# Kernel optimization log

Hardware: AMD Instinct MI355X
Metric: run time of the kernel (lower is better)

## Reference

```python
import jax, jax.numpy as jnp
import numpy as np

N_HEAD = 16


def _rope_tables(T, head_dim, dtype):
    # RotaryEmbedding buffers: freqs = outer(t, inv_freq), half-dim tables [T, head_dim//2]
    inv_freq = 1.0 / (10000.0 ** (jnp.arange(0, head_dim, 2, dtype=jnp.float32) / head_dim))
    freqs = jnp.arange(T, dtype=jnp.float32)[:, None] * inv_freq[None, :]
    return jnp.cos(freqs).astype(dtype), jnp.sin(freqs).astype(dtype)


def _apply_rotary(x, cos, sin):
    # x: [B,H,T,D]; cos/sin: [T,D//2] broadcast over B,H
    d = x.shape[-1] // 2
    x1, x2 = x[..., :d], x[..., d:]
    return jnp.concatenate([x1 * cos - x2 * sin, x2 * cos + x1 * sin], axis=-1)


def setup_inputs() -> dict:
    key = jax.random.key(0)
    k1, k2, k3 = jax.random.split(key, 3)
    B, T, C = 2, 2048, 2048
    x = jax.random.normal(k1, (B, T, C), dtype=jnp.float32)
    Wqkv = jax.random.normal(k2, (C, 3 * C), dtype=jnp.float32) * (1.0 / np.sqrt(C))
    Wproj = jax.random.normal(k3, (C, C), dtype=jnp.float32) * (1.0 / np.sqrt(C))
    return {"x": x, "Wqkv": Wqkv, "Wproj": Wproj}


def reference(x, Wqkv, Wproj):
    B, T, C = x.shape
    H = N_HEAD
    D = C // H
    qkv = (x @ Wqkv).reshape(B, T, 3, H, D)
    q, k, v = qkv[:, :, 0], qkv[:, :, 1], qkv[:, :, 2]  # [B,T,H,D]
    q = jnp.transpose(q, (0, 2, 1, 3))  # [B,H,T,D]
    k = jnp.transpose(k, (0, 2, 1, 3))
    v = jnp.transpose(v, (0, 2, 1, 3))
    cos, sin = _rope_tables(T, D, x.dtype)
    q = _apply_rotary(q, cos, sin)
    k = _apply_rotary(k, cos, sin)
    scale = 1.0 / np.sqrt(D)
    scores = jnp.einsum('bhqd,bhkd->bhqk', q, k) * scale
    causal = jnp.tril(jnp.ones((T, T), dtype=bool))
    scores = jnp.where(causal, scores, jnp.finfo(scores.dtype).min)
    attn = jax.nn.softmax(scores, axis=-1)
    out = jnp.einsum('bhqk,bhkd->bhqd', attn, v)
    out = jnp.transpose(out, (0, 2, 1, 3)).reshape(B, T, C)
    return out @ Wproj
```

## Files before the change

### kernel.cpp

```cpp
#include <hip/hip_runtime.h>
#include <hip/hip_bf16.h>

typedef short s16b;
using bf16x4 = __attribute__((ext_vector_type(4))) short;
using bf16x8 = __attribute__((ext_vector_type(8))) short;
using f32x4  = __attribute__((ext_vector_type(4))) float;

#define DEVINL __device__ __forceinline__

DEVINL float bf2f(short u) {
    union { float f; unsigned u; } x;
    x.u = ((unsigned)(unsigned short)u) << 16;
    return x.f;
}
DEVINL short f2bf(float f) {
    unsigned u = __builtin_bit_cast(unsigned, f);
    u += 0x7FFFu + ((u >> 16) & 1u);
    return (short)(u >> 16);
}

DEVINL f32x4 mfma16(bf16x8 a, bf16x8 b, f32x4 c) {
    return __builtin_amdgcn_mfma_f32_16x16x32_bf16(a, b, c, 0, 0, 0);
}

DEVINL void gload_lds16(const void* g, void* lds_uniform) {
    __builtin_amdgcn_global_load_lds(
        (const __attribute__((address_space(1))) char*)(const char*)g,
        (__attribute__((address_space(3))) char*)(char*)lds_uniform, 16, 0, 0);
}

DEVINL int perm32(int k) {
    return ((k >> 2) & 3) * 8 + ((k >> 4) & 1) * 4 + (k & 3);
}

DEVINL bf16x8 lds128(const s16b* base, int row, int ks, int g) {
    const char* p = (const char*)base + row * 128 + ((((ks << 2) + g) ^ (row & 7)) << 4);
    return *(const bf16x8*)p;
}
DEVINL bf16x8 lds256(const s16b* base, int row, int ds, int g) {
    const char* p = (const char*)base + row * 256 + ((((ds << 2) + g) ^ (row & 7)) << 4);
    return *(const bf16x8*)p;
}

__global__ void k_tables(float* __restrict__ ctab, float* __restrict__ stab) {
    int idx = blockIdx.x * 256 + threadIdx.x;
    int i = idx & 63, t = idx >> 6;
    float inv = powf(10000.0f, -(float)i * (1.0f / 64.0f));
    float fr = (float)t * inv;
    ctab[idx] = cosf(fr);
    stab[idx] = sinf(fr);
}

__global__ void k_cvt_x(const float* __restrict__ x, s16b* __restrict__ xb) {
    int idx = blockIdx.x * 256 + threadIdx.x;
    int p = idx * 4;
    int row = p >> 11, pc = p & 2047;
    int grp = pc >> 5, sp = pc & 31;
    int c = sp >> 3, half = (sp >> 2) & 1;
    int ksrc = grp * 32 + half * 16 + c * 4;
    float4 v = *(const float4*)(x + (size_t)row * 2048 + ksrc);
    bf16x4 o;
    o[0] = f2bf(v.x); o[1] = f2bf(v.y); o[2] = f2bf(v.z); o[3] = f2bf(v.w);
    *(bf16x4*)(xb + (size_t)row * 2048 + pc) = o;
}

__global__ void k_tcvt(const float* __restrict__ in, s16b* __restrict__ out, int R, int C) {
    __shared__ float tile[32][33];
    int tx = threadIdx.x & 31, ty = threadIdx.x >> 5;
    int c0 = blockIdx.x * 32, r0 = blockIdx.y * 32;
#pragma unroll
    for (int kk = 0; kk < 4; ++kk) {
        int r = ty + kk * 8;
        tile[r][tx] = in[(size_t)(r0 + r) * C + c0 + tx];
    }
    __syncthreads();
#pragma unroll
    for (int kk = 0; kk < 4; ++kk) {
        int r = ty + kk * 8;
        out[(size_t)(c0 + r) * R + r0 + perm32(tx)] = f2bf(tile[tx][r]);
    }
}

#define STG_B01(DB, KB)                                                        \
  gload_lds16(srcB + (KB), lds + 49152 + (DB) * 32768 + tid16);                \
  gload_lds16(srcB + 262144 + (KB), lds + 49152 + (DB) * 32768 + 8192 + tid16);
#define STG_B23(DB, KB)                                                        \
  gload_lds16(srcB + 524288 + (KB), lds + 49152 + (DB) * 32768 + 16384 + tid16); \
  gload_lds16(srcB + 786432 + (KB), lds + 49152 + (DB) * 32768 + 24576 + tid16);
#define STG_A01(DB, KB)                                                        \
  gload_lds16(srcA + (KB), lds + (DB) * 16384 + tid16);                        \
  gload_lds16(srcA + 262144 + (KB), lds + (DB) * 16384 + 8192 + tid16);

#define AF_READ(B, KS)                                                         \
    _Pragma("unroll")                                                          \
    for (int fi = 0; fi < 4; ++fi) {                                           \
      int row = (fi >> 1) * 64 + wm * 32 + (fi & 1) * 16 + r15;                \
      af[fi] = *(const bf16x8*)(lds + (B) * 16384 + row * 128                  \
               + ((((KS) * 4 + g) ^ (row & 7)) << 4));                         \
    }

#define PH4(B, KH, JH, STGC, WN)                                               \
  {                                                                            \
    if ((JH) == 0) { AF_READ(B, KH) }                                          \
    _Pragma("unroll")                                                          \
    for (int fj = 0; fj < 2; ++fj) {                                           \
      int row = (JH) * 128 + wn * 32 + fj * 16 + r15;                          \
      bfr[fj] = *(const bf16x8*)(lds + 49152 + (B) * 32768 + row * 128         \
                + ((((KH) * 4 + g) ^ (row & 7)) << 4));                        \
    }                                                                          \
    STGC                                                                       \
    if ((WN) == 6) { asm volatile("s_waitcnt vmcnt(6)" ::: "memory");          \
                     __builtin_amdgcn_sched_barrier(0); }                      \
    else if ((WN) == 0) { asm volatile("s_waitcnt vmcnt(0)" ::: "memory");     \
                     __builtin_amdgcn_sched_barrier(0); }                      \
    __builtin_amdgcn_s_barrier();                                              \
    asm volatile("s_waitcnt lgkmcnt(0)" ::: "memory");                         \
    __builtin_amdgcn_sched_barrier(0);                                         \
    __builtin_amdgcn_s_setprio(1);                                             \
    _Pragma("unroll")                                                          \
    for (int fi = 0; fi < 4; ++fi)                                             \
      _Pragma("unroll")                                                        \
      for (int fj = 0; fj < 2; ++fj)                                           \
        acc[fi][(JH) * 2 + fj] = mfma16(af[fi], bfr[fj], acc[fi][(JH) * 2 + fj]); \
    __builtin_amdgcn_s_setprio(0);                                             \
    __builtin_amdgcn_s_barrier();                                              \
    __builtin_amdgcn_sched_barrier(0);                                         \
  }

#define DO_TILE3(B, S1, S2, S3, WNL)                                           \
    PH4(B, 0, 0, S1, -1)                                                       \
    PH4(B, 0, 1, S2, -1)                                                       \
    PH4(B, 1, 0, S3, -1)                                                       \
    PH4(B, 1, 1, , WNL)

#define GEMM3_MAINLOOP(A_, B_)                                                 \
    __shared__ __attribute__((aligned(16))) char lds[147456];                  \
    const int tid = threadIdx.x;                                               \
    const int lane = tid & 63, wave = tid >> 6;                                \
    const int g = lane >> 4, r15 = lane & 15;                                  \
    const int wm = wave >> 2, wn = wave & 3;                                   \
    const int tid16 = tid << 4;                                                \
    const int rowL = tid16 >> 7;                                               \
    const int swzL = ((((tid16 >> 4) & 7) ^ (rowL & 7)) << 4);                 \
    const char* srcA = (const char*)(A_) + (size_t)(bm + rowL) * 4096 + swzL;  \
    const char* srcB = (const char*)(B_) + (size_t)(bn + rowL) * 4096 + swzL;  \
    f32x4 acc[4][4] = {};                                                      \
    bf16x8 af[4], bfr[2];                                                      \
    STG_B01(0, 0) STG_A01(0, 0) STG_B23(0, 0)                                  \
    STG_B01(1, 128) STG_A01(1, 128) STG_B23(1, 128)                            \
    asm volatile("s_waitcnt vmcnt(6)" ::: "memory");                           \
    __builtin_amdgcn_sched_barrier(0);                                         \
    __builtin_amdgcn_s_barrier();                                              \
    for (int t3 = 0; t3 < 10; ++t3) {                                          \
        const int kb2 = (3 * t3 + 2) * 128;                                    \
        const int kb3 = kb2 + 128, kb4 = kb2 + 256;                            \
        DO_TILE3(0, STG_B01(2, kb2), STG_A01(2, kb2), STG_B23(2, kb2), 6)      \
        DO_TILE3(1, STG_B01(0, kb3), STG_A01(0, kb3), STG_B23(0, kb3), 6)      \
        DO_TILE3(2, STG_B01(1, kb4), STG_A01(1, kb4), STG_B23(1, kb4), 6)      \
    }                                                                          \
    DO_TILE3(0, , , , 0)                                                       \
    DO_TILE3(1, , , , -1)

__global__ __launch_bounds__(512) void k_gemm_qkv(
    const s16b* __restrict__ A, const s16b* __restrict__ Bt,
    s16b* __restrict__ Qb, s16b* __restrict__ Kb, s16b* __restrict__ Vt) {
    const int bid = blockIdx.x;
    const int xcd = bid & 7, local = bid >> 3;
    const int rr_ = local >> 5, w = local & 31;
    const int bm = ((xcd & 3) * 8 + (w >> 2)) * 128;
    const int bn = ((xcd >> 2) * 12 + rr_ * 4 + (w & 3)) * 256;
    GEMM3_MAINLOOP(A, Bt)
    const int which = bn >> 11;
    if (which < 2) {
        s16b* dst = which ? Kb : Qb;
        char* sml = (char*)lds;
#pragma unroll
        for (int i = 0; i < 4; ++i) {
#pragma unroll
            for (int j = 0; j < 4; ++j) {
                int mb0 = (i >> 1) * 64 + wm * 32 + (i & 1) * 16 + 4 * g;
                int nn = (j >> 1) * 128 + wn * 32 + (j & 1) * 16 + r15;
#pragma unroll
                for (int e = 0; e < 4; ++e) {
                    int mm = mb0 + e;
                    *(s16b*)(sml + mm * 528 + ((nn * 2) ^ ((mm & 3) << 5))) =
                        f2bf(acc[i][j][e]);
                }
            }
        }
        __syncthreads();
        const int mrow = tid >> 2, c4 = tid & 3;
        const int bb = bm >> 11;
        const int tt = (bm & 2047) + mrow;
        const char* srow = sml + mrow * 528;
        const int sw = (mrow & 3) << 5;
#pragma unroll
        for (int k = 0; k < 8; ++k) {
            int lc = c4 + 4 * k;
            bf16x8 v = *(const bf16x8*)(srow + ((lc * 16) ^ sw));
            int ng = bn + lc * 8;
            int h = (ng >> 7) & 15, d = ng & 127;
            *(bf16x8*)(dst + ((size_t)(bb * 16 + h) * 2048 + tt) * 128 + d) = v;
        }
    } else {
#pragma unroll
        for (int i = 0; i < 4; ++i) {
            int m0 = bm + (i >> 1) * 64 + wm * 32 + (i & 1) * 16 + 4 * g;
            int b = m0 >> 11, t0 = m0 & 2047;
#pragma unroll
            for (int j = 0; j < 4; ++j) {
                int n = bn + (j >> 1) * 128 + wn * 32 + (j & 1) * 16 + r15;
                int h = (n >> 7) & 15, d = n & 127;
                size_t bh = (size_t)(b * 16 + h);
                int pt = (t0 & ~31) + perm32(t0 & 31);
                size_t base = (bh * 128 + d) * 2048 + pt;
                bf16x4 pk;
#pragma unroll
                for (int e = 0; e < 4; ++e) pk[e] = f2bf(acc[i][j][e]);
                *(bf16x4*)(Vt + base) = pk;
            }
        }
    }
}

__global__ __launch_bounds__(512) void k_gemm_proj(
    const s16b* __restrict__ A, const s16b* __restrict__ Bt, float* __restrict__ Co) {
    const int bid = blockIdx.x;
    const int xcd = bid & 7, local = bid >> 3;
    const int bm = (xcd * 4 + (local & 3)) * 128;
    const int bn = (local >> 2) * 256;
    GEMM3_MAINLOOP(A, Bt)
#pragma unroll
    for (int i = 0; i < 4; ++i) {
        int m0 = bm + (i >> 1) * 64 + wm * 32 + (i & 1) * 16 + 4 * g;
#pragma unroll
        for (int j = 0; j < 4; ++j) {
            int n = bn + (j >> 1) * 128 + wn * 32 + (j & 1) * 16 + r15;
#pragma unroll
            for (int e = 0; e < 4; ++e) Co[(size_t)(m0 + e) * 2048 + n] = acc[i][j][e];
        }
    }
}

__global__ void k_rope(s16b* __restrict__ Qb, const s16b* __restrict__ Kb,
                       s16b* __restrict__ Kp,
                       const float* __restrict__ ctab, const float* __restrict__ stab) {
    int idx = blockIdx.x * 256 + threadIdx.x;
    int i4 = idx & 15;
    int t = (idx >> 4) & 2047;
    int bh = (idx >> 15) & 31;
    int which = idx >> 20;
    int d = i4 * 4;
    const float* cp = ctab + t * 64 + d;
    const float* sp = stab + t * 64 + d;
    size_t rowoff = ((size_t)bh * 2048 + t) * 128;
    if (which == 0) {
        s16b* P = Qb + rowoff;
        bf16x4 a = *(bf16x4*)(P + d);
        bf16x4 bv = *(bf16x4*)(P + d + 64);
        bf16x4 ra, rb;
#pragma unroll
        for (int e = 0; e < 4; ++e) {
            float c = cp[e], s = sp[e];
            float x1 = bf2f(a[e]), x2 = bf2f(bv[e]);
            ra[e] = f2bf(x1 * c - x2 * s);
            rb[e] = f2bf(x2 * c + x1 * s);
        }
        *(bf16x4*)(P + d) = ra;
        *(bf16x4*)(P + d + 64) = rb;
    } else {
        const s16b* Pi = Kb + rowoff;
        s16b* Po = Kp + rowoff;
        bf16x4 a = *(const bf16x4*)(Pi + d);
        bf16x4 bv = *(const bf16x4*)(Pi + d + 64);
        bf16x4 ra, rb;
#pragma unroll
        for (int e = 0; e < 4; ++e) {
            float c = cp[e], s = sp[e];
            float x1 = bf2f(a[e]), x2 = bf2f(bv[e]);
            ra[e] = f2bf(x1 * c - x2 * s);
            rb[e] = f2bf(x2 * c + x1 * s);
        }
        int d2 = d + 64;
        int pd  = (d  & ~31) + perm32(d  & 31);
        int pd2 = (d2 & ~31) + perm32(d2 & 31);
        *(bf16x4*)(Po + pd) = ra;
        *(bf16x4*)(Po + pd2) = rb;
    }
}

__global__ __launch_bounds__(256) void k_attn(
    const s16b* __restrict__ Qb, const s16b* __restrict__ Kp,
    const s16b* __restrict__ Vt, s16b* __restrict__ AO) {
    __shared__ alignas(16) s16b Ks[64 * 128];
    __shared__ alignas(16) s16b Vs[128 * 64];
    const int tid = threadIdx.x;
    const int lane = tid & 63, wave = tid >> 6;
    const int g = lane >> 4, r15 = lane & 15;
    const int bh = blockIdx.x, qt = 15 - blockIdx.y;
    const int q0 = qt * 128 + wave * 32;
    const s16b* Qg = Qb + (size_t)bh * 2048 * 128;
    const char* Kg = (const char*)(Kp + (size_t)bh * 2048 * 128);
    const char* Vg = (const char*)(Vt + (size_t)bh * 128 * 2048);

    bf16x8 qf[2][4];
#pragma unroll
    for (int qs = 0; qs < 2; ++qs)
#pragma unroll
        for (int ds = 0; ds < 4; ++ds) {
            const s16b* p = Qg + (size_t)(q0 + qs * 16 + r15) * 128 + ds * 32 + 4 * g;
            bf16x4 lo = *(const bf16x4*)p;
            bf16x4 hi = *(const bf16x4*)(p + 16);
            qf[qs][ds] = __builtin_shufflevector(lo, hi, 0, 1, 2, 3, 4, 5, 6, 7);
        }

    f32x4 ot[8][2] = {};
    float m_s[2] = {-3e38f, -3e38f};
    float l_s[2] = {0.f, 0.f};
    const float scale = 0.0883883476483184f;

    const int ktiles = qt * 2 + 2;
    for (int kt = 0; kt < ktiles; ++kt) {
        const int k0 = kt * 64;
        __syncthreads();
#pragma unroll
        for (int rr = 0; rr < 4; ++rr) {
            int uo = (rr * 256 + wave * 64) * 16;
            int o = uo + lane * 16;
            {
                int row = o >> 8, sl = (o >> 4) & 15;
                int sg = (sl ^ (row & 7)) << 4;
                gload_lds16(Kg + (size_t)(k0 + row) * 256 + sg, (char*)Ks + uo);
            }
            {
                int row = o >> 7, sl = (o >> 4) & 7;
                int sg = (sl ^ (row & 7)) << 4;
                gload_lds16(Vg + (size_t)row * 4096 + (size_t)k0 * 2 + sg, (char*)Vs + uo);
            }
        }
        __syncthreads();

        if (k0 <= q0 + 31) {
            f32x4 st[4][2] = {};
            __builtin_amdgcn_s_setprio(1);
#pragma unroll
            for (int ds = 0; ds < 4; ++ds) {
#pragma unroll
                for (int ks = 0; ks < 4; ++ks) {
                    bf16x8 kf = lds256(Ks, ks * 16 + r15, ds, g);
#pragma unroll
                    for (int qs = 0; qs < 2; ++qs)
                        st[ks][qs] = mfma16(kf, qf[qs][ds], st[ks][qs]);
                }
            }
            __builtin_amdgcn_s_setprio(0);
#pragma unroll
            for (int ks = 0; ks < 4; ++ks)
#pragma unroll
                for (int qs = 0; qs < 2; ++qs)
#pragma unroll
                    for (int e = 0; e < 4; ++e) {
                        int kk = k0 + ks * 16 + 4 * g + e;
                        int qq = q0 + qs * 16 + r15;
                        float s = st[ks][qs][e] * scale;
                        st[ks][qs][e] = (kk <= qq) ? s : -3e38f;
                    }
            float sf[2];
#pragma unroll
            for (int qs = 0; qs < 2; ++qs) {
                float mx = -3e38f;
#pragma unroll
                for (int ks = 0; ks < 4; ++ks)
#pragma unroll
                    for (int e = 0; e < 4; ++e) mx = fmaxf(mx, st[ks][qs][e]);
                mx = fmaxf(mx, __shfl_xor(mx, 16));
                mx = fmaxf(mx, __shfl_xor(mx, 32));
                float mn = fmaxf(m_s[qs], mx);
                sf[qs] = __expf(m_s[qs] - mn);
                m_s[qs] = mn;
                float sum = 0.f;
#pragma unroll
                for (int ks = 0; ks < 4; ++ks)
#pragma unroll
                    for (int e = 0; e < 4; ++e) {
                        float p = __expf(st[ks][qs][e] - mn);
                        st[ks][qs][e] = p;
                        sum += p;
                    }
                sum += __shfl_xor(sum, 16);
                sum += __shfl_xor(sum, 32);
                l_s[qs] = l_s[qs] * sf[qs] + sum;
            }
            bf16x8 pb[2][2];
#pragma unroll
            for (int k2 = 0; k2 < 2; ++k2)
#pragma unroll
                for (int qs = 0; qs < 2; ++qs) {
                    bf16x8 f;
#pragma unroll
                    for (int jj = 0; jj < 8; ++jj)
                        f[jj] = f2bf(st[2 * k2 + (jj >> 2)][qs][jj & 3]);
                    pb[k2][qs] = f;
                }
#pragma unroll
            for (int d8 = 0; d8 < 8; ++d8)
#pragma unroll
                for (int qs = 0; qs < 2; ++qs)
#pragma unroll
                    for (int e = 0; e < 4; ++e) ot[d8][qs][e] *= sf[qs];
            __builtin_amdgcn_s_setprio(1);
#pragma unroll
            for (int k2 = 0; k2 < 2; ++k2)
#pragma unroll
                for (int d8 = 0; d8 < 8; ++d8) {
                    bf16x8 vf = lds128(Vs, d8 * 16 + r15, k2, g);
#pragma unroll
                    for (int qs = 0; qs < 2; ++qs)
                        ot[d8][qs] = mfma16(vf, pb[k2][qs], ot[d8][qs]);
                }
            __builtin_amdgcn_s_setprio(0);
        }
    }
    int b = bh >> 4, h = bh & 15;
#pragma unroll
    for (int qs = 0; qs < 2; ++qs) {
        float inv = 1.0f / l_s[qs];
        int q = q0 + qs * 16 + r15;
#pragma unroll
        for (int d8 = 0; d8 < 8; ++d8) {
            bf16x4 pk;
#pragma unroll
            for (int e = 0; e < 4; ++e) pk[e] = f2bf(ot[d8][qs][e] * inv);
            size_t off = ((size_t)(b * 2048 + q)) * 2048
                       + h * 128 + (d8 >> 1) * 32 + g * 8 + (d8 & 1) * 4;
            *(bf16x4*)(AO + off) = pk;
        }
    }
}

extern "C" void kernel_launch(void* const* d_in, const int* in_sizes, int n_in,
                              void* d_out, int out_size, void* d_ws, size_t ws_size,
                              hipStream_t stream) {
    const float* x = (const float*)d_in[0];
    const float* Wqkv = (const float*)d_in[1];
    const float* Wproj = (const float*)d_in[2];
    float* out = (float*)d_out;

    char* ws = (char*)d_ws;
    float* ctab = (float*)ws;
    float* stab = ctab + 2048 * 64;
    size_t off = 1048576;
    s16b* xb = (s16b*)(ws + off); off += 16777216;
    s16b* wqkvt = (s16b*)(ws + off); off += 25165824;
    s16b* wprojt = (s16b*)(ws + off); off += 8388608;
    s16b* Qb = (s16b*)(ws + off); off += 16777216;
    s16b* Kb = (s16b*)(ws + off); off += 16777216;
    s16b* Vt = (s16b*)(ws + off); off += 16777216;
    s16b* AO = xb;
    s16b* Kp = wqkvt;

    k_tables<<<dim3(512), dim3(256), 0, stream>>>(ctab, stab);
    k_cvt_x<<<dim3(8192), dim3(256), 0, stream>>>(x, xb);
    k_tcvt<<<dim3(192, 64), dim3(256), 0, stream>>>(Wqkv, wqkvt, 2048, 6144);
    k_tcvt<<<dim3(64, 64), dim3(256), 0, stream>>>(Wproj, wprojt, 2048, 2048);
    k_gemm_qkv<<<dim3(768), dim3(512), 0, stream>>>(xb, wqkvt, Qb, Kb, Vt);
    k_rope<<<dim3(8192), dim3(256), 0, stream>>>(Qb, Kb, Kp, ctab, stab);
    k_attn<<<dim3(32, 16), dim3(256), 0, stream>>>(Qb, Kp, Vt, AO);
    k_gemm_proj<<<dim3(256), dim3(512), 0, stream>>>(AO, wprojt, out);
}
```

Before: 270.2 us.

## Rewrite QKV GEMM with 256x256 tiles, double-buffered LDS and phased MFMA

Replaces the QKV projection GEMM's 128x256 triple-buffered mainloop with a dedicated 256x256 tile kernel. Each wave now holds an 8x4 accumulator, and loads are staged in quarter-tile phases with explicit waitcnt, barriers and setprio around MFMA bursts. The grid shrinks to 384 blocks with a new XCD-aware tile mapping, and the epilogues are adapted to the larger tile. The aim is higher arithmetic intensity and less global/LDS traffic per FLOP. The cost is about 132KB of LDS, heavy register pressure, only two LDS buffers, and fewer blocks (384 over 256 CUs), which risks tail imbalance.

```diff
diff --git a/kernel.cpp b/kernel.cpp
--- a/kernel.cpp
+++ b/kernel.cpp
@@ -78,6 +78,147 @@
     for (int kk = 0; kk < 4; ++kk) {
         int r = ty + kk * 8;
         out[(size_t)(c0 + r) * R + r0 + perm32(tx)] = f2bf(tile[tx][r]);
+    }
+}
+
+#define QSTG_A0(DB, KB)                                                        \
+  gload_lds16(srcA + (KB), lds + (DB) * 32768 + tid16);                        \
+  gload_lds16(srcA + 262144 + (KB), lds + (DB) * 32768 + 8192 + tid16);
+#define QSTG_A1(DB, KB)                                                        \
+  gload_lds16(srcA + 524288 + (KB), lds + (DB) * 32768 + 16384 + tid16);       \
+  gload_lds16(srcA + 786432 + (KB), lds + (DB) * 32768 + 24576 + tid16);
+#define QSTG_B0(DB, KB)                                                        \
+  gload_lds16(srcB + (KB), lds + 65536 + (DB) * 32768 + tid16);                \
+  gload_lds16(srcB + 262144 + (KB), lds + 65536 + (DB) * 32768 + 8192 + tid16);
+#define QSTG_B1(DB, KB)                                                        \
+  gload_lds16(srcB + 524288 + (KB), lds + 65536 + (DB) * 32768 + 16384 + tid16); \
+  gload_lds16(srcB + 786432 + (KB), lds + 65536 + (DB) * 32768 + 24576 + tid16);
+
+#define QPH(B, KS, NH, RDAF, STGC, WN)                                         \
+  {                                                                            \
+    if (RDAF) {                                                                \
+      _Pragma("unroll")                                                        \
+      for (int fi = 0; fi < 8; ++fi) {                                         \
+        int row = wm * 128 + fi * 16 + r15;                                    \
+        af[fi] = *(const bf16x8*)(lds + (B) * 32768 + row * 128                \
+                 + ((((KS) * 4 + g) ^ (row & 7)) << 4));                       \
+      }                                                                        \
+    }                                                                          \
+    _Pragma("unroll")                                                          \
+    for (int fj = 0; fj < 2; ++fj) {                                           \
+      int row = (NH) * 128 + wn * 32 + fj * 16 + r15;                          \
+      bfr[fj] = *(const bf16x8*)(lds + 65536 + (B) * 32768 + row * 128         \
+                + ((((KS) * 4 + g) ^ (row & 7)) << 4));                        \
+    }                                                                          \
+    STGC                                                                       \
+    if ((WN) == 4) { asm volatile("s_waitcnt vmcnt(4)" ::: "memory");          \
+                     __builtin_amdgcn_sched_barrier(0); }                      \
+    else if ((WN) == 2) { asm volatile("s_waitcnt vmcnt(2)" ::: "memory");     \
+                     __builtin_amdgcn_sched_barrier(0); }                      \
+    else if ((WN) == 0) { asm volatile("s_waitcnt vmcnt(0)" ::: "memory");     \
+                     __builtin_amdgcn_sched_barrier(0); }                      \
+    __builtin_amdgcn_s_barrier();                                              \
+    asm volatile("s_waitcnt lgkmcnt(0)" ::: "memory");                         \
+    __builtin_amdgcn_sched_barrier(0);                                         \
+    __builtin_amdgcn_s_setprio(1);                                             \
+    _Pragma("unroll")                                                          \
+    for (int fi = 0; fi < 8; ++fi)                                             \
+      _Pragma("unroll")                                                        \
+      for (int fj = 0; fj < 2; ++fj)                                           \
+        acc[fi][(NH) * 2 + fj] = mfma16(af[fi], bfr[fj], acc[fi][(NH) * 2 + fj]); \
+    __builtin_amdgcn_s_setprio(0);                                             \
+    __builtin_amdgcn_s_barrier();                                              \
+    __builtin_amdgcn_sched_barrier(0);                                         \
+  }
+
+#define QTILE(B, KB)                                                           \
+  QPH(B, 0, 0, 1, QSTG_A0(1 - (B), KB) QSTG_B0(1 - (B), KB), 4)                \
+  QPH(B, 0, 1, 0, QSTG_A1(1 - (B), KB), -1)                                    \
+  QPH(B, 1, 0, 1, QSTG_B1(1 - (B), KB), -1)                                    \
+  QPH(B, 1, 1, 0, , 2)
+#define QTILE_LAST(B)                                                          \
+  QPH(B, 0, 0, 1, , 0) QPH(B, 0, 1, 0, , -1)                                   \
+  QPH(B, 1, 0, 1, , -1) QPH(B, 1, 1, 0, , -1)
+
+__global__ __launch_bounds__(512) void k_gemm_qkv(
+    const s16b* __restrict__ A, const s16b* __restrict__ Bt,
+    s16b* __restrict__ Qb, s16b* __restrict__ Kb, s16b* __restrict__ Vt) {
+    __shared__ __attribute__((aligned(16))) char lds[135168];
+    const int bid = blockIdx.x;
+    const int xcd = bid & 7, local = bid >> 3;
+    const int bm = ((xcd & 1) * 8 + (local & 7)) * 256;
+    const int bn = ((xcd >> 1) * 6 + (local >> 3)) * 256;
+    const int tid = threadIdx.x;
+    const int lane = tid & 63, wave = tid >> 6;
+    const int g = lane >> 4, r15 = lane & 15;
+    const int wm = wave >> 2, wn = wave & 3;
+    const int tid16 = tid << 4;
+    const int rowL = tid16 >> 7;
+    const int swzL = ((((tid16 >> 4) & 7) ^ (rowL & 7)) << 4);
+    const char* srcA = (const char*)A + (size_t)(bm + rowL) * 4096 + swzL;
+    const char* srcB = (const char*)Bt + (size_t)(bn + rowL) * 4096 + swzL;
+    f32x4 acc[8][4] = {};
+    bf16x8 af[8], bfr[2];
+
+    QSTG_A0(0, 0) QSTG_B0(0, 0) QSTG_A1(0, 0) QSTG_B1(0, 0)
+    asm volatile("s_waitcnt vmcnt(2)" ::: "memory");
+    __builtin_amdgcn_sched_barrier(0);
+    __builtin_amdgcn_s_barrier();
+    for (int t2 = 0; t2 < 15; ++t2) {
+        const int kb1 = (2 * t2 + 1) * 128, kb2 = kb1 + 128;
+        QTILE(0, kb1)
+        QTILE(1, kb2)
+    }
+    QTILE(0, 3968)
+    QTILE_LAST(1)
+
+    const int which = bn >> 11;
+    if (which < 2) {
+        s16b* dst = which ? Kb : Qb;
+        char* sml = (char*)lds;
+#pragma unroll
+        for (int fi = 0; fi < 8; ++fi) {
+#pragma unroll
+            for (int nq = 0; nq < 4; ++nq) {
+                int nn = (nq >> 1) * 128 + wn * 32 + (nq & 1) * 16 + r15;
+#pragma unroll
+                for (int e = 0; e < 4; ++e) {
+                    int mm = wm * 128 + fi * 16 + 4 * g + e;
+                    *(s16b*)(sml + mm * 528 + ((nn * 2) ^ ((mm & 3) << 5))) =
+                        f2bf(acc[fi][nq][e]);
+                }
+            }
+        }
+        __syncthreads();
+        const int mrow = tid >> 1, half = tid & 1;
+        const int bb = bm >> 11, tt = (bm & 2047) + mrow;
+        const char* srow = sml + mrow * 528;
+        const int sw = (mrow & 3) << 5;
+#pragma unroll
+        for (int k = 0; k < 16; ++k) {
+            int c = half * 16 + k;
+            bf16x8 v = *(const bf16x8*)(srow + ((c * 16) ^ sw));
+            int ng = bn + c * 8;
+            int h = (ng >> 7) & 15, d = ng & 127;
+            *(bf16x8*)(dst + ((size_t)(bb * 16 + h) * 2048 + tt) * 128 + d) = v;
+        }
+    } else {
+#pragma unroll
+        for (int fi = 0; fi < 8; ++fi) {
+            int m0 = bm + wm * 128 + fi * 16 + 4 * g;
+            int b = m0 >> 11, t0 = m0 & 2047;
+            int pt = (t0 & ~31) + perm32(t0 & 31);
+#pragma unroll
+            for (int nq = 0; nq < 4; ++nq) {
+                int n = bn + (nq >> 1) * 128 + wn * 32 + (nq & 1) * 16 + r15;
+                int h = (n >> 7) & 15, d = n & 127;
+                size_t base = ((size_t)(b * 16 + h) * 128 + d) * 2048 + pt;
+                bf16x4 pk;
+#pragma unroll
+                for (int e = 0; e < 4; ++e) pk[e] = f2bf(acc[fi][nq][e]);
+                *(bf16x4*)(Vt + base) = pk;
+            }
+        }
     }
 }
 
@@ -161,68 +302,6 @@
     DO_TILE3(0, , , , 0)                                                       \
     DO_TILE3(1, , , , -1)
 
-__global__ __launch_bounds__(512) void k_gemm_qkv(
-    const s16b* __restrict__ A, const s16b* __restrict__ Bt,
-    s16b* __restrict__ Qb, s16b* __restrict__ Kb, s16b* __restrict__ Vt) {
-    const int bid = blockIdx.x;
-    const int xcd = bid & 7, local = bid >> 3;
-    const int rr_ = local >> 5, w = local & 31;
-    const int bm = ((xcd & 3) * 8 + (w >> 2)) * 128;
-    const int bn = ((xcd >> 2) * 12 + rr_ * 4 + (w & 3)) * 256;
-    GEMM3_MAINLOOP(A, Bt)
-    const int which = bn >> 11;
-    if (which < 2) {
-        s16b* dst = which ? Kb : Qb;
-        char* sml = (char*)lds;
-#pragma unroll
-        for (int i = 0; i < 4; ++i) {
-#pragma unroll
-            for (int j = 0; j < 4; ++j) {
-                int mb0 = (i >> 1) * 64 + wm * 32 + (i & 1) * 16 + 4 * g;
-                int nn = (j >> 1) * 128 + wn * 32 + (j & 1) * 16 + r15;
-#pragma unroll
-                for (int e = 0; e < 4; ++e) {
-                    int mm = mb0 + e;
-                    *(s16b*)(sml + mm * 528 + ((nn * 2) ^ ((mm & 3) << 5))) =
-                        f2bf(acc[i][j][e]);
-                }
-            }
-        }
-        __syncthreads();
-        const int mrow = tid >> 2, c4 = tid & 3;
-        const int bb = bm >> 11;
-        const int tt = (bm & 2047) + mrow;
-        const char* srow = sml + mrow * 528;
-        const int sw = (mrow & 3) << 5;
-#pragma unroll
-        for (int k = 0; k < 8; ++k) {
-            int lc = c4 + 4 * k;
-            bf16x8 v = *(const bf16x8*)(srow + ((lc * 16) ^ sw));
-            int ng = bn + lc * 8;
-            int h = (ng >> 7) & 15, d = ng & 127;
-            *(bf16x8*)(dst + ((size_t)(bb * 16 + h) * 2048 + tt) * 128 + d) = v;
-        }
-    } else {
-#pragma unroll
-        for (int i = 0; i < 4; ++i) {
-            int m0 = bm + (i >> 1) * 64 + wm * 32 + (i & 1) * 16 + 4 * g;
-            int b = m0 >> 11, t0 = m0 & 2047;
-#pragma unroll
-            for (int j = 0; j < 4; ++j) {
-                int n = bn + (j >> 1) * 128 + wn * 32 + (j & 1) * 16 + r15;
-                int h = (n >> 7) & 15, d = n & 127;
-                size_t bh = (size_t)(b * 16 + h);
-                int pt = (t0 & ~31) + perm32(t0 & 31);
-                size_t base = (bh * 128 + d) * 2048 + pt;
-                bf16x4 pk;
-#pragma unroll
-                for (int e = 0; e < 4; ++e) pk[e] = f2bf(acc[i][j][e]);
-                *(bf16x4*)(Vt + base) = pk;
-            }
-        }
-    }
-}
-
 __global__ __launch_bounds__(512) void k_gemm_proj(
     const s16b* __restrict__ A, const s16b* __restrict__ Bt, float* __restrict__ Co) {
     const int bid = blockIdx.x;
@@ -463,7 +542,7 @@
     k_cvt_x<<<dim3(8192), dim3(256), 0, stream>>>(x, xb);
     k_tcvt<<<dim3(192, 64), dim3(256), 0, stream>>>(Wqkv, wqkvt, 2048, 6144);
     k_tcvt<<<dim3(64, 64), dim3(256), 0, stream>>>(Wproj, wprojt, 2048, 2048);
-    k_gemm_qkv<<<dim3(768), dim3(512), 0, stream>>>(xb, wqkvt, Qb, Kb, Vt);
+    k_gemm_qkv<<<dim3(384), dim3(512), 0, stream>>>(xb, wqkvt, Qb, Kb, Vt);
     k_rope<<<dim3(8192), dim3(256), 0, stream>>>(Qb, Kb, Kp, ctab, stab);
     k_attn<<<dim3(32, 16), dim3(256), 0, stream>>>(Qb, Kp, Vt, AO);
     k_gemm_proj<<<dim3(256), dim3(512), 0, stream>>>(AO, wprojt, out);
```

Measured after the change: 284.3 us. 5.2% more time.
